# Kernel tuning notes

Measured on AMD Instinct MI355X. Metric: run time of the kernel, lower is better.

## Reference

```python
import jax, jax.numpy as jnp
import numpy as np

NODE_DIM = 256
EDGE_DIM = 128
NODE_IN = 768 + 769 + 4 + 1 + 3  # 1545


def setup_inputs() -> dict:
    key = jax.random.key(0)
    ks = jax.random.split(key, 16)
    B, N, H, W, C = 8, 128, 128, 128, 768
    obj_feats = jax.random.normal(ks[0], (B, N, 769), dtype=jnp.float32)
    masks = jax.random.uniform(ks[1], (B, N, H, W), dtype=jnp.float32)
    features = jax.random.normal(ks[2], (B, C, H, W), dtype=jnp.float32)
    bboxes = jax.random.uniform(ks[3], (B, N, 4), dtype=jnp.float32)
    conf = jax.random.uniform(ks[4], (B, N), dtype=jnp.float32)
    depth = jax.random.uniform(ks[5], (B, 1, H, W), dtype=jnp.float32) + 0.1
    # near-identity pose so homogeneous divide is well-conditioned
    pose = jnp.eye(4, dtype=jnp.float32)[None] + 0.01 * jax.random.normal(ks[6], (B, 4, 4), dtype=jnp.float32)
    s = 0.02
    node_w1 = s * jax.random.normal(ks[7], (512, NODE_IN), dtype=jnp.float32)
    node_b1 = jnp.zeros((512,), dtype=jnp.float32)
    node_w2 = s * jax.random.normal(ks[8], (NODE_DIM, 512), dtype=jnp.float32)
    node_b2 = jnp.zeros((NODE_DIM,), dtype=jnp.float32)
    edge_w1 = s * jax.random.normal(ks[9], (256, 2 * NODE_DIM), dtype=jnp.float32)
    edge_b1 = jnp.zeros((256,), dtype=jnp.float32)
    edge_w2 = s * jax.random.normal(ks[10], (EDGE_DIM, 256), dtype=jnp.float32)
    edge_b2 = jnp.zeros((EDGE_DIM,), dtype=jnp.float32)
    return dict(obj_feats=obj_feats, masks=masks, features=features, bboxes=bboxes,
                conf=conf, depth=depth, pose=pose,
                node_w1=node_w1, node_b1=node_b1, node_w2=node_w2, node_b2=node_b2,
                edge_w1=edge_w1, edge_b1=edge_b1, edge_w2=edge_w2, edge_b2=edge_b2)


def _forward(obj_feats, masks, features, bboxes, conf, depth, pose,
             node_w1, node_b1, node_w2, node_b2,
             edge_w1, edge_b1, edge_w2, edge_b2):
    B, C, H, W = features.shape
    N = masks.shape[1]
    K = jnp.eye(3, dtype=features.dtype)  # self.intrinsics

    # --- mask pooling: normalized mask-weighted average of features ---
    feats_flat = features.reshape(B, C, H * W)                 # [B,C,HW]
    m_flat = masks.reshape(B, N, H * W)                        # [B,N,HW]
    m_norm = m_flat / (m_flat.sum(-1, keepdims=True) + 1e-6)
    pooled = jnp.einsum('bnh,bch->bnc', m_norm, feats_flat)    # [B,N,C]

    # --- positional encoding ---
    x1, y1, x2, y2 = bboxes[..., 0], bboxes[..., 1], bboxes[..., 2], bboxes[..., 3]
    pos_feat = jnp.stack([(x1 + x2) / 2, (y1 + y2) / 2, x2 - x1, y2 - y1], axis=-1)  # [B,N,4]

    # --- motion prior ---
    ys = jnp.arange(H, dtype=masks.dtype)
    xs = jnp.arange(W, dtype=masks.dtype)
    mask_sum = masks.sum((-1, -2)) + 1e-6                      # [B,N]
    cx = jnp.einsum('bnhw,w->bn', masks, xs) / mask_sum
    cy = jnp.einsum('bnhw,h->bn', masks, ys) / mask_sum
    cx_idx = jnp.clip(jnp.round(cx).astype(jnp.int32), 0, W - 1)
    cy_idx = jnp.clip(jnp.round(cy).astype(jnp.int32), 0, H - 1)
    b_idx = jnp.arange(B)[:, None]                             # [B,1]
    z = depth[b_idx, 0, cy_idx, cx_idx]                        # [B,N]
    X = (cx - K[0, 2]) * z / K[0, 0]
    Y = (cy - K[1, 2]) * z / K[1, 1]
    ones = jnp.ones_like(z)
    P_h = jnp.stack([X, Y, z, ones], axis=-1)                  # [B,N,4]
    P_next = jnp.einsum('bij,bnj->bni', pose, P_h)             # [B,N,4]
    motion = P_next[..., :3] / P_next[..., 3:]                 # [B,N,3]

    # --- node MLP ---
    node_input = jnp.concatenate([pooled, obj_feats, pos_feat, conf[..., None], motion], axis=-1)
    h = jax.nn.relu(node_input @ node_w1.T + node_b1)
    node_emb = h @ node_w2.T + node_b2                         # [B,N,node_dim]

    # --- edge MLP: cat([n_i, n_j]) @ W1 == n_i @ W1a + n_j @ W1b (avoid O(N^2 * 2D) cat) ---
    D = node_emb.shape[-1]
    w1a, w1b = edge_w1[:, :D], edge_w1[:, D:]
    hi = node_emb @ w1a.T                                      # [B,N,256]
    hj = node_emb @ w1b.T                                      # [B,N,256]
    he = jax.nn.relu(hi[:, :, None, :] + hj[:, None, :, :] + edge_b1)  # [B,N,N,256]
    edge_emb = he @ edge_w2.T + edge_b2                        # [B,N,N,edge_dim]

    # --- adjacency: exp(-cdist) ---
    sq = jnp.sum(node_emb * node_emb, axis=-1)                 # [B,N]
    d2 = sq[:, :, None] + sq[:, None, :] - 2.0 * jnp.einsum('bnd,bmd->bnm', node_emb, node_emb)
    d2 = jnp.maximum(d2, 0.0)
    d = jnp.where(d2 > 0, jnp.sqrt(jnp.where(d2 > 0, d2, 1.0)), 0.0)  # grad-safe sqrt at 0
    adj = jnp.exp(-d)
    return node_emb, edge_emb, adj


def reference(obj_feats, masks, features, bboxes, conf, depth, pose,
              node_w1, node_b1, node_w2, node_b2,
              edge_w1, edge_b1, edge_w2, edge_b2):
    return _forward(obj_feats, masks, features, bboxes, conf, depth, pose,
                    node_w1, node_b1, node_w2, node_b2,
                    edge_w1, edge_b1, edge_w2, edge_b2)
```

## Files before the change

kernel.cpp:

```cpp
#include <hip/hip_runtime.h>
#include <hip/hip_bf16.h>

#define B_   8
#define N_   128
#define HW_  16384
#define C_   768
#define NIN_ 1545
#define NINP_ 1600
#define D1_  512
#define D_   256
#define EO_  128

typedef short s16x8 __attribute__((ext_vector_type(8)));
typedef float f32x16 __attribute__((ext_vector_type(16)));

__device__ __forceinline__ unsigned short f2bf(float x) {
  union { __hip_bfloat16 h; unsigned short u; } cv;
  cv.h = __float2bfloat16(x);
  return cv.u;
}

__global__ __launch_bounds__(256) void mask_stats_k(const float* __restrict__ masks,
                                                    const float* __restrict__ depth,
                                                    const float* __restrict__ pose,
                                                    float4* __restrict__ stats) {
  int row = blockIdx.x;
  int b = row >> 7;
  const float4* mp = (const float4*)(masks + (size_t)row * HW_);
  double s = 0.0, sx = 0.0, sy = 0.0;
  for (int it = 0; it < 16; ++it) {
    int i4 = threadIdx.x + it * 256;
    float4 v = mp[i4];
    int flat = i4 * 4;
    int y = flat >> 7, xb = flat & 127;
    double rs = (double)v.x + (double)v.y + (double)v.z + (double)v.w;
    s += rs;
    sx += (double)v.x * xb + (double)v.y * (xb + 1) + (double)v.z * (xb + 2) + (double)v.w * (xb + 3);
    sy += rs * (double)y;
  }
  for (int off = 32; off; off >>= 1) {
    s  += __shfl_down(s,  off);
    sx += __shfl_down(sx, off);
    sy += __shfl_down(sy, off);
  }
  __shared__ double red[3][4];
  int w = threadIdx.x >> 6, l = threadIdx.x & 63;
  if (l == 0) { red[0][w] = s; red[1][w] = sx; red[2][w] = sy; }
  __syncthreads();
  if (threadIdx.x == 0) {
    s  = red[0][0] + red[0][1] + red[0][2] + red[0][3];
    sx = red[1][0] + red[1][1] + red[1][2] + red[1][3];
    sy = red[2][0] + red[2][1] + red[2][2] + red[2][3];
    double msum = s + 1e-6;
    double cx = sx / msum, cy = sy / msum;
    int cxi = (int)rint(cx); cxi = min(127, max(0, cxi));
    int cyi = (int)rint(cy); cyi = min(127, max(0, cyi));
    double z = (double)depth[(size_t)b * HW_ + cyi * 128 + cxi];
    double Ph[4] = { cx * z, cy * z, z, 1.0 };
    const float* P = pose + b * 16;
    double pn[4];
    #pragma unroll
    for (int r = 0; r < 4; ++r)
      pn[r] = (double)P[r*4+0]*Ph[0] + (double)P[r*4+1]*Ph[1] + (double)P[r*4+2]*Ph[2] + (double)P[r*4+3]*Ph[3];
    double inv3 = 1.0 / pn[3];
    stats[row] = make_float4((float)(1.0 / msum), (float)(pn[0]*inv3), (float)(pn[1]*inv3), (float)(pn[2]*inv3));
  }
}

__global__ __launch_bounds__(256) void convw_k(const float* __restrict__ w1,
                                               const float* __restrict__ w2,
                                               const float* __restrict__ ew1,
                                               const float* __restrict__ ew2,
                                               unsigned short* __restrict__ w1b,
                                               unsigned short* __restrict__ w2b,
                                               unsigned short* __restrict__ we1b,
                                               unsigned short* __restrict__ ew2b) {
  int i = blockIdx.x * 256 + threadIdx.x;
  if (i < 512 * NINP_) {
    int r = i / NINP_, k = i - r * NINP_;
    w1b[i] = f2bf(k < NIN_ ? w1[r * NIN_ + k] : 0.0f);
    return;
  }
  i -= 512 * NINP_;
  if (i < 256 * 512) { w2b[i] = f2bf(w2[i]); return; }
  i -= 256 * 512;
  if (i < 512 * 256) {
    int r = i >> 8, k = i & 255;
    we1b[i] = f2bf(r < 256 ? ew1[r * 512 + k] : ew1[(r - 256) * 512 + 256 + k]);
    return;
  }
  i -= 512 * 256;
  if (i < 128 * 256) { ew2b[i] = f2bf(ew2[i]); }
}

__global__ __launch_bounds__(256) void pooled_k(const float* __restrict__ masks,
                                                const float* __restrict__ feats,
                                                float* __restrict__ Spart) {
  __shared__ short As[128 * 72];
  __shared__ short Bs[128 * 72];
  int bx = blockIdx.x;
  int ct = bx % 6, kc = bx / 6;
  int b = blockIdx.y;
  const float* mb = masks + (size_t)b * N_ * HW_;
  const float* fb = feats + ((size_t)b * C_ + (size_t)ct * 128) * HW_;
  int t = threadIdx.x, w = t >> 6, l = t & 63;
  int rsel = l & 31, khalf = l >> 5;
  f32x16 acc[4];
  #pragma unroll
  for (int nt = 0; nt < 4; ++nt)
    #pragma unroll
    for (int i = 0; i < 16; ++i) acc[nt][i] = 0.0f;

  for (int kt = 0; kt < 32; ++kt) {
    int kbase = kc * 2048 + kt * 64;
    #pragma unroll
    for (int c = 0; c < 8; ++c) {
      int chunk = t + 256 * c;
      int row = chunk >> 4;
      int kof = (chunk & 15) << 2;
      float4 va = *(const float4*)(mb + (size_t)row * HW_ + kbase + kof);
      ushort4 pa = { f2bf(va.x), f2bf(va.y), f2bf(va.z), f2bf(va.w) };
      *(ushort4*)((unsigned short*)As + row * 72 + kof) = pa;
      float4 vb = *(const float4*)(fb + (size_t)row * HW_ + kbase + kof);
      ushort4 pb = { f2bf(vb.x), f2bf(vb.y), f2bf(vb.z), f2bf(vb.w) };
      *(ushort4*)((unsigned short*)Bs + row * 72 + kof) = pb;
    }
    __syncthreads();
    #pragma unroll
    for (int ks = 0; ks < 4; ++ks) {
      s16x8 a = *(const s16x8*)&As[(w * 32 + rsel) * 72 + ks * 16 + khalf * 8];
      #pragma unroll
      for (int nt = 0; nt < 4; ++nt) {
        s16x8 bf = *(const s16x8*)&Bs[(nt * 32 + rsel) * 72 + ks * 16 + khalf * 8];
        acc[nt] = __builtin_amdgcn_mfma_f32_32x32x16_bf16(a, bf, acc[nt], 0, 0, 0);
      }
    }
    __syncthreads();
  }
  float* op = Spart + (size_t)kc * (B_ * N_ * C_ / 8 * 8) / 8 * 8;
  op = Spart + (size_t)kc * 786432 + (size_t)b * 98304;
  #pragma unroll
  for (int nt = 0; nt < 4; ++nt)
    #pragma unroll
    for (int reg = 0; reg < 16; ++reg) {
      int rm = w * 32 + (reg & 3) + 8 * (reg >> 2) + 4 * khalf;
      int cn = ct * 128 + nt * 32 + rsel;
      op[rm * C_ + cn] = acc[nt][reg];
    }
}

__global__ __launch_bounds__(256) void assemble_k(const float* __restrict__ Spart,
                                                  const float4* __restrict__ stats,
                                                  const float* __restrict__ obj,
                                                  const float* __restrict__ bboxes,
                                                  const float* __restrict__ conf,
                                                  unsigned short* __restrict__ ni) {
  int r = blockIdx.x;
  float4 st = stats[r];
  float x1 = bboxes[r*4+0], y1 = bboxes[r*4+1], x2 = bboxes[r*4+2], y2 = bboxes[r*4+3];
  for (int k = threadIdx.x; k < NINP_; k += 256) {
    float v;
    if (k < 768) {
      float acc = 0.0f;
      #pragma unroll
      for (int kc = 0; kc < 8; ++kc) acc += Spart[(size_t)kc * 786432 + (size_t)r * C_ + k];
      v = acc * st.x;
    } else if (k < 1537) v = obj[(size_t)r * 769 + (k - 768)];
    else if (k == 1537) v = 0.5f * (x1 + x2);
    else if (k == 1538) v = 0.5f * (y1 + y2);
    else if (k == 1539) v = x2 - x1;
    else if (k == 1540) v = y2 - y1;
    else if (k == 1541) v = conf[r];
    else if (k == 1542) v = st.y;
    else if (k == 1543) v = st.z;
    else if (k == 1544) v = st.w;
    else v = 0.0f;
    ni[(size_t)r * NINP_ + k] = f2bf(v);
  }
}

template <bool RELU, bool BIAS, int OUTM>
__global__ __launch_bounds__(256) void gemm64_k(const unsigned short* __restrict__ A,
                                                const unsigned short* __restrict__ Bm,
                                                const float* __restrict__ bias,
                                                float* __restrict__ Cf,
                                                unsigned short* __restrict__ Cb,
                                                int K, int N) {
  __shared__ short As[64 * 72];
  __shared__ short Bs[64 * 72];
  int n0 = blockIdx.x * 64, m0 = blockIdx.y * 64;
  int t = threadIdx.x, w = t >> 6, l = t & 63;
  int rsel = l & 31, khalf = l >> 5;
  int mh = (w & 1) * 32, nh = (w >> 1) * 32;
  f32x16 acc;
  #pragma unroll
  for (int i = 0; i < 16; ++i) acc[i] = 0.0f;

  for (int k0 = 0; k0 < K; k0 += 64) {
    #pragma unroll
    for (int c = 0; c < 2; ++c) {
      int chunk = t + 256 * c;
      int row = chunk >> 3, kof = (chunk & 7) * 8;
      *(uint4*)((unsigned short*)As + row * 72 + kof) =
          *(const uint4*)&A[(size_t)(m0 + row) * K + k0 + kof];
      *(uint4*)((unsigned short*)Bs + row * 72 + kof) =
          *(const uint4*)&Bm[(size_t)(n0 + row) * K + k0 + kof];
    }
    __syncthreads();
    #pragma unroll
    for (int ks = 0; ks < 4; ++ks) {
      s16x8 a = *(const s16x8*)&As[(mh + rsel) * 72 + ks * 16 + khalf * 8];
      s16x8 bf = *(const s16x8*)&Bs[(nh + rsel) * 72 + ks * 16 + khalf * 8];
      acc = __builtin_amdgcn_mfma_f32_32x32x16_bf16(a, bf, acc, 0, 0, 0);
    }
    __syncthreads();
  }
  #pragma unroll
  for (int reg = 0; reg < 16; ++reg) {
    int rm = m0 + mh + (reg & 3) + 8 * (reg >> 2) + 4 * khalf;
    int cn = n0 + nh + rsel;
    float v = acc[reg];
    if (BIAS) v += bias[cn];
    if (RELU) v = fmaxf(v, 0.0f);
    if (OUTM == 0 || OUTM == 2) Cf[(size_t)rm * N + cn] = v;
    if (OUTM == 1 || OUTM == 2) Cb[(size_t)rm * N + cn] = f2bf(v);
  }
}

__global__ __launch_bounds__(256) void edge_k(const float* __restrict__ hihj,
                                              const unsigned short* __restrict__ ew2b,
                                              const float* __restrict__ eb1,
                                              const float* __restrict__ eb2,
                                              float* __restrict__ out_edge) {
  __shared__ short W2s[128 * 264];
  __shared__ float hi_s[256];
  __shared__ float b1_s[256];
  __shared__ float b2_s[128];
  int bi = blockIdx.x;
  int b = bi >> 7;
  int t = threadIdx.x, w = t >> 6, l = t & 63;
  int rsel = l & 31, khalf = l >> 5;

  #pragma unroll
  for (int c = 0; c < 16; ++c) {
    int chunk = t + 256 * c;
    int row = chunk >> 5, kof = (chunk & 31) * 8;
    *(uint4*)((unsigned short*)W2s + row * 264 + kof) = *(const uint4*)&ew2b[row * 256 + kof];
  }
  hi_s[t] = hihj[(size_t)bi * 512 + t];
  b1_s[t] = eb1[t];
  if (t < 128) b2_s[t] = eb2[t];
  __syncthreads();

  f32x16 acc[4];
  #pragma unroll
  for (int nt = 0; nt < 4; ++nt)
    #pragma unroll
    for (int i = 0; i < 16; ++i) acc[nt][i] = 0.0f;

  const float* hjb = hihj + (size_t)b * 128 * 512 + 256;
  int jrow = w * 32 + rsel;
  #pragma unroll
  for (int ks = 0; ks < 16; ++ks) {
    int k0 = ks * 16 + khalf * 8;
    const float* hp = hjb + (size_t)jrow * 512 + k0;
    float4 h0 = *(const float4*)hp;
    float4 h1 = *(const float4*)(hp + 4);
    float f[8] = { h0.x, h0.y, h0.z, h0.w, h1.x, h1.y, h1.z, h1.w };
    s16x8 a;
    #pragma unroll
    for (int c = 0; c < 8; ++c)
      a[c] = (short)f2bf(fmaxf(f[c] + hi_s[k0 + c] + b1_s[k0 + c], 0.0f));
    #pragma unroll
    for (int nt = 0; nt < 4; ++nt) {
      s16x8 bf = *(const s16x8*)&W2s[(nt * 32 + rsel) * 264 + k0];
      acc[nt] = __builtin_amdgcn_mfma_f32_32x32x16_bf16(a, bf, acc[nt], 0, 0, 0);
    }
  }
  float* ob = out_edge + (size_t)bi * 128 * 128;
  #pragma unroll
  for (int nt = 0; nt < 4; ++nt)
    #pragma unroll
    for (int reg = 0; reg < 16; ++reg) {
      int j = w * 32 + (reg & 3) + 8 * (reg >> 2) + 4 * khalf;
      int o = nt * 32 + rsel;
      ob[(size_t)j * 128 + o] = acc[nt][reg] + b2_s[o];
    }
}

__global__ __launch_bounds__(128) void adj_k(const float* __restrict__ ne,
                                             float* __restrict__ adj) {
  int bi = blockIdx.x;
  int b = bi >> 7;
  __shared__ float nei[256];
  int t = threadIdx.x;
  nei[t] = ne[(size_t)bi * 256 + t];
  nei[t + 128] = ne[(size_t)bi * 256 + t + 128];
  __syncthreads();
  const float* nj = ne + ((size_t)b * 128 + t) * 256;
  float dot = 0.0f, sqj = 0.0f, sqi = 0.0f;
  for (int k = 0; k < 256; ++k) {
    float a = nei[k], c = nj[k];
    dot += a * c; sqj += c * c; sqi += a * a;
  }
  float d2 = fmaxf(sqi + sqj - 2.0f * dot, 0.0f);
  float d = d2 > 0.0f ? sqrtf(d2) : 0.0f;
  adj[(size_t)bi * 128 + t] = expf(-d);
}

extern "C" void kernel_launch(void* const* d_in, const int* in_sizes, int n_in,
                              void* d_out, int out_size, void* d_ws, size_t ws_size,
                              hipStream_t stream) {
  const float* obj    = (const float*)d_in[0];
  const float* masks  = (const float*)d_in[1];
  const float* feats  = (const float*)d_in[2];
  const float* bboxes = (const float*)d_in[3];
  const float* conf   = (const float*)d_in[4];
  const float* depth  = (const float*)d_in[5];
  const float* pose   = (const float*)d_in[6];
  const float* nw1    = (const float*)d_in[7];
  const float* nb1    = (const float*)d_in[8];
  const float* nw2    = (const float*)d_in[9];
  const float* nb2    = (const float*)d_in[10];
  const float* ew1    = (const float*)d_in[11];
  const float* eb1    = (const float*)d_in[12];
  const float* ew2    = (const float*)d_in[13];
  const float* eb2    = (const float*)d_in[14];

  char* ws = (char*)d_ws;
  float*          Spart = (float*)ws;
  unsigned short* h_bf  = (unsigned short*)ws;
  unsigned short* ne_bf = (unsigned short*)(ws + 1048576);
  float*          hihj  = (float*)(ws + 1572864);
  float4*         stats = (float4*)(ws + 25165824);
  unsigned short* ni_bf = (unsigned short*)(ws + 25182208);
  unsigned short* w1b   = (unsigned short*)(ws + 28459008);
  unsigned short* w2b   = (unsigned short*)(ws + 30097408);
  unsigned short* we1b  = (unsigned short*)(ws + 30359552);
  unsigned short* ew2b  = (unsigned short*)(ws + 30621696);

  float* out      = (float*)d_out;
  float* out_ne   = out;
  float* out_edge = out + 262144;
  float* out_adj  = out + 262144 + 16777216;

  mask_stats_k<<<dim3(1024), dim3(256), 0, stream>>>(masks, depth, pose, stats);
  convw_k<<<dim3(4352), dim3(256), 0, stream>>>(nw1, nw2, ew1, ew2, w1b, w2b, we1b, ew2b);
  pooled_k<<<dim3(48, 8), dim3(256), 0, stream>>>(masks, feats, Spart);
  assemble_k<<<dim3(1024), dim3(256), 0, stream>>>(Spart, stats, obj, bboxes, conf, ni_bf);
  gemm64_k<true,  true,  1><<<dim3(8, 16), dim3(256), 0, stream>>>(ni_bf, w1b, nb1, nullptr, h_bf, NINP_, 512);
  gemm64_k<false, true,  2><<<dim3(4, 16), dim3(256), 0, stream>>>(h_bf, w2b, nb2, out_ne, ne_bf, 512, 256);
  gemm64_k<false, false, 0><<<dim3(8, 16), dim3(256), 0, stream>>>(ne_bf, we1b, nullptr, hihj, nullptr, 256, 512);
  edge_k<<<dim3(1024), dim3(256), 0, stream>>>(hihj, ew2b, eb1, eb2, out_edge);
  adj_k<<<dim3(1024), dim3(128), 0, stream>>>(out_ne, out_adj);
}
```

Baseline: 729.8 us.

## Pre-convert masks to bf16 in stats pass and widen pooled C tile

The mask statistics kernel now also writes a bf16 copy of the masks. The pooling GEMM reads that copy instead of re-reading and converting the fp32 masks for every channel tile. The pooling tile now covers 256 channels instead of 128, so masks are re-read 3 times rather than 6, and K is split into 16 chunks instead of 8. This cuts global memory traffic in the bandwidth-bound pooling step. In exchange it adds an extra 32MB bf16 write, doubles the partial-sum buffer that assemble must reduce, and raises LDS use per block.

```diff
diff --git a/kernel.cpp b/kernel.cpp
--- a/kernel.cpp
+++ b/kernel.cpp
@@ -7,9 +7,6 @@
 #define C_   768
 #define NIN_ 1545
 #define NINP_ 1600
-#define D1_  512
-#define D_   256
-#define EO_  128
 
 typedef short s16x8 __attribute__((ext_vector_type(8)));
 typedef float f32x16 __attribute__((ext_vector_type(16)));
@@ -23,14 +20,18 @@
 __global__ __launch_bounds__(256) void mask_stats_k(const float* __restrict__ masks,
                                                     const float* __restrict__ depth,
                                                     const float* __restrict__ pose,
-                                                    float4* __restrict__ stats) {
+                                                    float4* __restrict__ stats,
+                                                    unsigned short* __restrict__ mbf) {
   int row = blockIdx.x;
   int b = row >> 7;
   const float4* mp = (const float4*)(masks + (size_t)row * HW_);
+  unsigned short* mb = mbf + (size_t)row * HW_;
   double s = 0.0, sx = 0.0, sy = 0.0;
   for (int it = 0; it < 16; ++it) {
     int i4 = threadIdx.x + it * 256;
     float4 v = mp[i4];
+    ushort4 pv = { f2bf(v.x), f2bf(v.y), f2bf(v.z), f2bf(v.w) };
+    *(ushort4*)(mb + i4 * 4) = pv;
     int flat = i4 * 4;
     int y = flat >> 7, xb = flat & 127;
     double rs = (double)v.x + (double)v.y + (double)v.z + (double)v.w;
@@ -93,59 +94,61 @@
   if (i < 128 * 256) { ew2b[i] = f2bf(ew2[i]); }
 }
 
-__global__ __launch_bounds__(256) void pooled_k(const float* __restrict__ masks,
+__global__ __launch_bounds__(256) void pooled_k(const unsigned short* __restrict__ masks_bf,
                                                 const float* __restrict__ feats,
                                                 float* __restrict__ Spart) {
   __shared__ short As[128 * 72];
-  __shared__ short Bs[128 * 72];
-  int bx = blockIdx.x;
-  int ct = bx % 6, kc = bx / 6;
+  __shared__ short Bs[256 * 72];
+  int kc = blockIdx.x & 15;
+  int cg = blockIdx.x >> 4;
   int b = blockIdx.y;
-  const float* mb = masks + (size_t)b * N_ * HW_;
-  const float* fb = feats + ((size_t)b * C_ + (size_t)ct * 128) * HW_;
+  const unsigned short* mb = masks_bf + (size_t)b * N_ * HW_;
+  const float* fb = feats + ((size_t)b * C_ + (size_t)cg * 256) * HW_;
   int t = threadIdx.x, w = t >> 6, l = t & 63;
   int rsel = l & 31, khalf = l >> 5;
   f32x16 acc[4];
   #pragma unroll
-  for (int nt = 0; nt < 4; ++nt)
-    #pragma unroll
-    for (int i = 0; i < 16; ++i) acc[nt][i] = 0.0f;
-
-  for (int kt = 0; kt < 32; ++kt) {
-    int kbase = kc * 2048 + kt * 64;
-    #pragma unroll
-    for (int c = 0; c < 8; ++c) {
+  for (int mt = 0; mt < 4; ++mt)
+    #pragma unroll
+    for (int i = 0; i < 16; ++i) acc[mt][i] = 0.0f;
+
+  for (int kt = 0; kt < 16; ++kt) {
+    int kbase = kc * 1024 + kt * 64;
+    #pragma unroll
+    for (int c = 0; c < 4; ++c) {
       int chunk = t + 256 * c;
-      int row = chunk >> 4;
-      int kof = (chunk & 15) << 2;
-      float4 va = *(const float4*)(mb + (size_t)row * HW_ + kbase + kof);
-      ushort4 pa = { f2bf(va.x), f2bf(va.y), f2bf(va.z), f2bf(va.w) };
-      *(ushort4*)((unsigned short*)As + row * 72 + kof) = pa;
-      float4 vb = *(const float4*)(fb + (size_t)row * HW_ + kbase + kof);
-      ushort4 pb = { f2bf(vb.x), f2bf(vb.y), f2bf(vb.z), f2bf(vb.w) };
-      *(ushort4*)((unsigned short*)Bs + row * 72 + kof) = pb;
+      int row = chunk >> 3, kof = (chunk & 7) * 8;
+      *(uint4*)((unsigned short*)As + row * 72 + kof) =
+          *(const uint4*)(mb + (size_t)row * HW_ + kbase + kof);
+    }
+    #pragma unroll
+    for (int c = 0; c < 16; ++c) {
+      int chunk = t + 256 * c;
+      int row = chunk >> 4, kof = (chunk & 15) * 4;
+      float4 v = *(const float4*)(fb + (size_t)row * HW_ + kbase + kof);
+      ushort4 pv = { f2bf(v.x), f2bf(v.y), f2bf(v.z), f2bf(v.w) };
+      *(ushort4*)((unsigned short*)Bs + row * 72 + kof) = pv;
     }
     __syncthreads();
     #pragma unroll
     for (int ks = 0; ks < 4; ++ks) {
-      s16x8 a = *(const s16x8*)&As[(w * 32 + rsel) * 72 + ks * 16 + khalf * 8];
+      s16x8 bf = *(const s16x8*)&Bs[(w * 32 + rsel) * 72 + ks * 16 + khalf * 8];
       #pragma unroll
-      for (int nt = 0; nt < 4; ++nt) {
-        s16x8 bf = *(const s16x8*)&Bs[(nt * 32 + rsel) * 72 + ks * 16 + khalf * 8];
-        acc[nt] = __builtin_amdgcn_mfma_f32_32x32x16_bf16(a, bf, acc[nt], 0, 0, 0);
+      for (int mt = 0; mt < 4; ++mt) {
+        s16x8 a = *(const s16x8*)&As[(mt * 32 + rsel) * 72 + ks * 16 + khalf * 8];
+        acc[mt] = __builtin_amdgcn_mfma_f32_32x32x16_bf16(a, bf, acc[mt], 0, 0, 0);
       }
     }
     __syncthreads();
   }
-  float* op = Spart + (size_t)kc * (B_ * N_ * C_ / 8 * 8) / 8 * 8;
-  op = Spart + (size_t)kc * 786432 + (size_t)b * 98304;
-  #pragma unroll
-  for (int nt = 0; nt < 4; ++nt)
+  float* op = Spart + (size_t)kc * 786432 + (size_t)b * 128 * 768;
+  #pragma unroll
+  for (int mt = 0; mt < 4; ++mt)
     #pragma unroll
     for (int reg = 0; reg < 16; ++reg) {
-      int rm = w * 32 + (reg & 3) + 8 * (reg >> 2) + 4 * khalf;
-      int cn = ct * 128 + nt * 32 + rsel;
-      op[rm * C_ + cn] = acc[nt][reg];
+      int rm = mt * 32 + (reg & 3) + 8 * (reg >> 2) + 4 * khalf;
+      int cn = cg * 256 + w * 32 + rsel;
+      op[(size_t)rm * 768 + cn] = acc[mt][reg];
     }
 }
 
@@ -163,7 +166,7 @@
     if (k < 768) {
       float acc = 0.0f;
       #pragma unroll
-      for (int kc = 0; kc < 8; ++kc) acc += Spart[(size_t)kc * 786432 + (size_t)r * C_ + k];
+      for (int kc = 0; kc < 16; ++kc) acc += Spart[(size_t)kc * 786432 + (size_t)r * 768 + k];
       v = acc * st.x;
     } else if (k < 1537) v = obj[(size_t)r * 769 + (k - 768)];
     else if (k == 1537) v = 0.5f * (x1 + x2);
@@ -328,25 +331,26 @@
   const float* eb2    = (const float*)d_in[14];
 
   char* ws = (char*)d_ws;
-  float*          Spart = (float*)ws;
-  unsigned short* h_bf  = (unsigned short*)ws;
-  unsigned short* ne_bf = (unsigned short*)(ws + 1048576);
-  float*          hihj  = (float*)(ws + 1572864);
-  float4*         stats = (float4*)(ws + 25165824);
-  unsigned short* ni_bf = (unsigned short*)(ws + 25182208);
-  unsigned short* w1b   = (unsigned short*)(ws + 28459008);
-  unsigned short* w2b   = (unsigned short*)(ws + 30097408);
-  unsigned short* we1b  = (unsigned short*)(ws + 30359552);
-  unsigned short* ew2b  = (unsigned short*)(ws + 30621696);
+  float*          Spart    = (float*)ws;
+  unsigned short* h_bf     = (unsigned short*)ws;
+  unsigned short* ne_bf    = (unsigned short*)(ws + 1048576);
+  float*          hihj     = (float*)(ws + 1572864);
+  unsigned short* masks_bf = (unsigned short*)(ws + 50331648);
+  float4*         stats    = (float4*)(ws + 83886080);
+  unsigned short* ni_bf    = (unsigned short*)(ws + 83902464);
+  unsigned short* w1b      = (unsigned short*)(ws + 87179264);
+  unsigned short* w2b      = (unsigned short*)(ws + 88817664);
+  unsigned short* we1b     = (unsigned short*)(ws + 89079808);
+  unsigned short* ew2b     = (unsigned short*)(ws + 89341952);
 
   float* out      = (float*)d_out;
   float* out_ne   = out;
   float* out_edge = out + 262144;
   float* out_adj  = out + 262144 + 16777216;
 
-  mask_stats_k<<<dim3(1024), dim3(256), 0, stream>>>(masks, depth, pose, stats);
+  mask_stats_k<<<dim3(1024), dim3(256), 0, stream>>>(masks, depth, pose, stats, masks_bf);
   convw_k<<<dim3(4352), dim3(256), 0, stream>>>(nw1, nw2, ew1, ew2, w1b, w2b, we1b, ew2b);
-  pooled_k<<<dim3(48, 8), dim3(256), 0, stream>>>(masks, feats, Spart);
+  pooled_k<<<dim3(48, 8), dim3(256), 0, stream>>>(masks_bf, feats, Spart);
   assemble_k<<<dim3(1024), dim3(256), 0, stream>>>(Spart, stats, obj, bboxes, conf, ni_bf);
   gemm64_k<true,  true,  1><<<dim3(8, 16), dim3(256), 0, stream>>>(ni_bf, w1b, nb1, nullptr, h_bf, NINP_, 512);
   gemm64_k<false, true,  2><<<dim3(4, 16), dim3(256), 0, stream>>>(h_bf, w2b, nb2, out_ne, ne_bf, 512, 256);
```

Result: slower. 797.6 us (+9.3%).
